# Performance work log

Hardware: AMD Instinct MI355X
Metric: run time of the kernel (lower is better)

The kernel has to match this reference:

```python
import jax, jax.numpy as jnp
import numpy as np

B, NUM_HIDDENS, H, W = 32, 128, 64, 64
EMB_DIM = 64
NUM_EMB = 512
COMMITMENT_COST = 0.25


def setup_inputs() -> dict:
    key = jax.random.key(0)
    ks = jax.random.split(key, 5)
    return {
        "bottom_encoding": jax.random.normal(ks[0], (B, NUM_HIDDENS, H, W), jnp.float32),
        "pre_w": jax.random.normal(ks[1], (EMB_DIM, NUM_HIDDENS), jnp.float32) / np.sqrt(NUM_HIDDENS).astype(np.float32),
        "pre_b": jnp.zeros((EMB_DIM,), jnp.float32),
        "codebook": jax.random.uniform(ks[2], (NUM_EMB, EMB_DIM), jnp.float32, -1.0 / NUM_EMB, 1.0 / NUM_EMB),
        "post_w": jax.random.normal(ks[3], (NUM_HIDDENS, EMB_DIM), jnp.float32) / np.sqrt(EMB_DIM).astype(np.float32),
        "post_b": jnp.zeros((NUM_HIDDENS,), jnp.float32),
    }


def reference(bottom_encoding, pre_w, pre_b, codebook, post_w, post_b):
    # pre-VQ 1x1 conv: [B, num_hiddens, H, W] -> [B, emb_dim, H, W]
    x = jnp.einsum('bchw,oc->bohw', bottom_encoding, pre_w) + pre_b[None, :, None, None]
    # BCHW -> BHWC, flatten to [N, D]
    z = jnp.transpose(x, (0, 2, 3, 1))
    flat = z.reshape(-1, EMB_DIM)
    # squared euclidean distances to codebook: [N, K]
    dists = (jnp.sum(flat * flat, axis=1, keepdims=True)
             + jnp.sum(codebook * codebook, axis=1)[None, :]
             - 2.0 * flat @ codebook.T)
    idx = jnp.argmin(dists, axis=1)              # [N] int
    quantized = codebook[idx].reshape(z.shape)   # gather, [B, H, W, D]
    # VQ losses
    e_latent_loss = jnp.mean((jax.lax.stop_gradient(quantized) - z) ** 2)
    q_latent_loss = jnp.mean((quantized - jax.lax.stop_gradient(z)) ** 2)
    loss = q_latent_loss + COMMITMENT_COST * e_latent_loss
    # straight-through estimator
    quantized_st = z + jax.lax.stop_gradient(quantized - z)
    # perplexity of codebook usage
    counts = jnp.zeros((NUM_EMB,), jnp.float32).at[idx].add(1.0)
    avg_probs = counts / idx.shape[0]
    perplexity = jnp.exp(-jnp.sum(avg_probs * jnp.log(avg_probs + 1e-10)))
    # post-VQ 1x1 conv: [B, emb_dim, H, W] -> [B, num_hiddens, H, W]
    qc = jnp.transpose(quantized_st, (0, 3, 1, 2))
    global_decode = jnp.einsum('bchw,oc->bohw', qc, post_w) + post_b[None, :, None, None]
    indices = idx.reshape(B, H, W)
    return loss, global_decode, perplexity, indices
```

## Files before the change

kernel.cpp:

```cpp
#include <hip/hip_runtime.h>

typedef unsigned short u16;
typedef unsigned int u32;
typedef __attribute__((ext_vector_type(8))) short short8v;
typedef __attribute__((ext_vector_type(4))) float f32x4;

#define NPX   131072
#define CHN   128
#define HWN   4096
#define EMB   64
#define NCODE 512

#define WS_HIST 0
#define WS_LOSS 2048
#define WS_CC   4096
#define WS_PWT  8192
#define WS_IDX  40960
#define WS_DT   303104


#define MFMA(a, b, c) __builtin_amdgcn_mfma_f32_16x16x32_bf16((a), (b), (c), 0, 0, 0)

#define SPLIT3(V, HH, MM, LL) {                          \
  u32 zb_ = __float_as_uint(V);                          \
  HH = zb_ >> 16;                                        \
  float fh_ = __uint_as_float(HH << 16);                 \
  float r1_ = __fsub_rn((V), fh_);                       \
  MM = __float_as_uint(r1_) >> 16;                       \
  float fm_ = __uint_as_float(MM << 16);                 \
  float r2_ = __fsub_rn(r1_, fm_);                       \
  LL = __float_as_uint(r2_) >> 16; }

__device__ __forceinline__ float rec3(u32 hb, u32 mb, u32 lb) {
  return __fadd_rn(__fadd_rn(__uint_as_float(hb), __uint_as_float(mb)),
                   __uint_as_float(lb));
}

__global__ __launch_bounds__(512) void vq_prep(const float* __restrict__ preW,
                                               const float* __restrict__ cb,
                                               float* __restrict__ preWT,
                                               float* __restrict__ cc,
                                               u16* __restrict__ ch,
                                               u16* __restrict__ cm,
                                               u16* __restrict__ cl) {
  int t = threadIdx.x;
  for (int i = t; i < CHN * EMB; i += 512) {
    int c = i >> 6, d = i & 63;
    preWT[i] = preW[d * CHN + c];
  }
  if (t < NCODE) {
    const float* row = cb + t * EMB;
    float r[8];
#pragma unroll
    for (int j = 0; j < 8; ++j) r[j] = __fmul_rn(row[j], row[j]);
#pragma unroll
    for (int b = 1; b < 8; ++b)
#pragma unroll
      for (int j = 0; j < 8; ++j)
        r[j] = __fadd_rn(r[j], __fmul_rn(row[b * 8 + j], row[b * 8 + j]));
    cc[t] = __fadd_rn(__fadd_rn(__fadd_rn(r[0], r[1]), __fadd_rn(r[2], r[3])),
                      __fadd_rn(__fadd_rn(r[4], r[5]), __fadd_rn(r[6], r[7])));
    int tile = t >> 4, rr = t & 15;
    for (int d = 0; d < EMB; ++d) {
      float v = row[d];
      u32 hh, mm, ll;
      SPLIT3(v, hh, mm, ll)
      size_t ti = (size_t)tile * 1024 + (size_t)(d >> 3) * 128 + rr * 8 + (d & 7);
      ch[ti] = (u16)hh;
      cm[ti] = (u16)mm;
      cl[ti] = (u16)ll;
    }
  }
}

__global__ __launch_bounds__(256) void vq_dtab(const float* __restrict__ cb,
                                               const float* __restrict__ postW,
                                               const float* __restrict__ postB,
                                               float* __restrict__ DT) {
  int idx = blockIdx.x * 256 + threadIdx.x;
  int k = idx >> 7, o = idx & 127;
  const float* q = cb + k * EMB;
  const float* w = postW + o * EMB;
  float a0 = 0.f, a1 = 0.f, a2 = 0.f, a3 = 0.f;
#pragma unroll
  for (int dd = 0; dd < 64; dd += 4) {
    a0 = fmaf(q[dd + 0], w[dd + 0], a0);
    a1 = fmaf(q[dd + 1], w[dd + 1], a1);
    a2 = fmaf(q[dd + 2], w[dd + 2], a2);
    a3 = fmaf(q[dd + 3], w[dd + 3], a3);
  }
  DT[(size_t)k * 128 + o] = ((a0 + a1) + (a2 + a3)) + postB[o];
}

__global__ __launch_bounds__(256) void vq_pre(const float* __restrict__ A,
                                              const float* __restrict__ preWT,
                                              const float* __restrict__ preB,
                                              u16* __restrict__ zh,
                                              u16* __restrict__ zm,
                                              u16* __restrict__ zl) {
  int bid = blockIdx.x;
  int ph = bid & 511, dh = bid >> 9;
  int d0 = dh << 5;
  int p = ph * 256 + threadIdx.x;
  int b = p >> 12, hw = p & 4095;
  const float* Ab = A + (size_t)b * CHN * HWN + hw;

  float z[32];
#pragma unroll
  for (int d = 0; d < 32; ++d) z[d] = 0.f;
  for (int c = 0; c < CHN; c += 4) {
    float a0 = Ab[(size_t)(c + 0) * HWN];
    float a1 = Ab[(size_t)(c + 1) * HWN];
    float a2 = Ab[(size_t)(c + 2) * HWN];
    float a3 = Ab[(size_t)(c + 3) * HWN];
    const float* w = preWT + c * EMB + d0;
#pragma unroll
    for (int d = 0; d < 32; ++d) z[d] = __fadd_rn(z[d], __fmul_rn(a0, w[d]));
    w += EMB;
#pragma unroll
    for (int d = 0; d < 32; ++d) z[d] = __fadd_rn(z[d], __fmul_rn(a1, w[d]));
    w += EMB;
#pragma unroll
    for (int d = 0; d < 32; ++d) z[d] = __fadd_rn(z[d], __fmul_rn(a2, w[d]));
    w += EMB;
#pragma unroll
    for (int d = 0; d < 32; ++d) z[d] = __fadd_rn(z[d], __fmul_rn(a3, w[d]));
  }
#pragma unroll
  for (int d = 0; d < 32; ++d) z[d] = __fadd_rn(z[d], preB[d0 + d]);

  u32 hwd[16], mwd[16], lwd[16];
#pragma unroll
  for (int i = 0; i < 32; ++i) {
    u32 hh, mm, ll;
    SPLIT3(z[i], hh, mm, ll)
    int wdi = i >> 1;
    if ((i & 1) == 0) { hwd[wdi] = hh; mwd[wdi] = mm; lwd[wdi] = ll; }
    else { hwd[wdi] |= hh << 16; mwd[wdi] |= mm << 16; lwd[wdi] |= ll << 16; }
  }
  int tile = p >> 4, rr = p & 15;
  size_t base = (size_t)tile * 1024 + (size_t)(dh * 4) * 128 + rr * 8;
#pragma unroll
  for (int q = 0; q < 4; ++q) {
    size_t off = base + (size_t)q * 128;
    *(uint4*)(zh + off) = make_uint4(hwd[4*q], hwd[4*q+1], hwd[4*q+2], hwd[4*q+3]);
    *(uint4*)(zm + off) = make_uint4(mwd[4*q], mwd[4*q+1], mwd[4*q+2], mwd[4*q+3]);
    *(uint4*)(zl + off) = make_uint4(lwd[4*q], lwd[4*q+1], lwd[4*q+2], lwd[4*q+3]);
  }
}

__global__ __launch_bounds__(256) void vq_zz(const u16* __restrict__ zh,
                                             const u16* __restrict__ zm,
                                             const u16* __restrict__ zl,
                                             float* __restrict__ zz) {
  int p = blockIdx.x * 256 + threadIdx.x;
  int tile = p >> 4, rr = p & 15;
  size_t base = (size_t)tile * 1024 + rr * 8;
  float r[8];
#pragma unroll
  for (int bb = 0; bb < 8; ++bb) {
    size_t off = base + (size_t)bb * 128;
    uint4 h4 = *(const uint4*)(zh + off);
    uint4 m4 = *(const uint4*)(zm + off);
    uint4 l4 = *(const uint4*)(zl + off);
    float zv[8];
    zv[0] = rec3(h4.x << 16, m4.x << 16, l4.x << 16);
    zv[1] = rec3(h4.x & 0xffff0000u, m4.x & 0xffff0000u, l4.x & 0xffff0000u);
    zv[2] = rec3(h4.y << 16, m4.y << 16, l4.y << 16);
    zv[3] = rec3(h4.y & 0xffff0000u, m4.y & 0xffff0000u, l4.y & 0xffff0000u);
    zv[4] = rec3(h4.z << 16, m4.z << 16, l4.z << 16);
    zv[5] = rec3(h4.z & 0xffff0000u, m4.z & 0xffff0000u, l4.z & 0xffff0000u);
    zv[6] = rec3(h4.w << 16, m4.w << 16, l4.w << 16);
    zv[7] = rec3(h4.w & 0xffff0000u, m4.w & 0xffff0000u, l4.w & 0xffff0000u);
#pragma unroll
    for (int j = 0; j < 8; ++j) {
      float sq = __fmul_rn(zv[j], zv[j]);
      r[j] = (bb == 0) ? sq : __fadd_rn(r[j], sq);
    }
  }
  zz[p] = __fadd_rn(__fadd_rn(__fadd_rn(r[0], r[1]), __fadd_rn(r[2], r[3])),
                    __fadd_rn(__fadd_rn(r[4], r[5]), __fadd_rn(r[6], r[7])));
}


#define LOADB(S, T) {                                                   \
  size_t ob_ = (size_t)((T) & 31) * 1024 + l8;                          \
  S##h0 = *(const short8v*)(ch + ob_); S##h1 = *(const short8v*)(ch + ob_ + 512); \
  S##m0 = *(const short8v*)(cm + ob_); S##m1 = *(const short8v*)(cm + ob_ + 512); \
  S##l0 = *(const short8v*)(cl + ob_); S##l1 = *(const short8v*)(cl + ob_ + 512); }

#define COMP(S, T) {                                                    \
  float ccv_ = scc[((T) << 4) + mcol];                                  \
  _Pragma("unroll")                                                     \
  for (int mt = 0; mt < 4; ++mt) {                                      \
    f32x4 acc = {0.f, 0.f, 0.f, 0.f};                                   \
    acc = MFMA(Ah[mt][0], S##h0, acc); acc = MFMA(Ah[mt][1], S##h1, acc); \
    acc = MFMA(Am[mt][0], S##h0, acc); acc = MFMA(Am[mt][1], S##h1, acc); \
    acc = MFMA(Ah[mt][0], S##m0, acc); acc = MFMA(Ah[mt][1], S##m1, acc); \
    acc = MFMA(Am[mt][0], S##m0, acc); acc = MFMA(Am[mt][1], S##m1, acc); \
    acc = MFMA(Al[mt][0], S##h0, acc); acc = MFMA(Al[mt][1], S##h1, acc); \
    acc = MFMA(Ah[mt][0], S##l0, acc); acc = MFMA(Ah[mt][1], S##l1, acc); \
    acc = MFMA(Al[mt][0], S##m0, acc); acc = MFMA(Al[mt][1], S##m1, acc); \
    acc = MFMA(Am[mt][0], S##l0, acc); acc = MFMA(Am[mt][1], S##l1, acc); \
    _Pragma("unroll")                                                   \
    for (int r = 0; r < 4; ++r) {                                       \
      float dist_ = __fadd_rn(__fadd_rn(zzr[mt][r], ccv_), -2.0f * acc[r]); \
      if (dist_ < best[mt][r]) { best[mt][r] = dist_; bidx[mt][r] = ((T) << 4) + mcol; } \
    } } }

__global__ __launch_bounds__(256, 2) void vq_search(const u16* __restrict__ zh,
                                                    const u16* __restrict__ zm,
                                                    const u16* __restrict__ zl,
                                                    const u16* __restrict__ ch,
                                                    const u16* __restrict__ cm,
                                                    const u16* __restrict__ cl,
                                                    const float* __restrict__ cc,
                                                    const float* __restrict__ zz,
                                                    u16* __restrict__ wsIdx) {
  __shared__ float scc[512];
  int tid = threadIdx.x;
  scc[tid] = cc[tid];
  scc[tid + 256] = cc[tid + 256];
  __syncthreads();

  int lane = tid & 63, wid = tid >> 6;
  int Mbase = blockIdx.x * 256 + wid * 64;
  int mcol = lane & 15, g = lane >> 4;
  size_t l8 = (size_t)lane * 8;

  short8v Ah[4][2], Am[4][2], Al[4][2];
#pragma unroll
  for (int mt = 0; mt < 4; ++mt) {
    size_t tz = (size_t)((Mbase >> 4) + mt) * 1024 + l8;
    Ah[mt][0] = *(const short8v*)(zh + tz); Ah[mt][1] = *(const short8v*)(zh + tz + 512);
    Am[mt][0] = *(const short8v*)(zm + tz); Am[mt][1] = *(const short8v*)(zm + tz + 512);
    Al[mt][0] = *(const short8v*)(zl + tz); Al[mt][1] = *(const short8v*)(zl + tz + 512);
  }
  float zzr[4][4];
#pragma unroll
  for (int mt = 0; mt < 4; ++mt)
#pragma unroll
    for (int r = 0; r < 4; ++r)
      zzr[mt][r] = zz[Mbase + mt * 16 + g * 4 + r];

  float best[4][4];
  int bidx[4][4];
#pragma unroll
  for (int mt = 0; mt < 4; ++mt)
#pragma unroll
    for (int r = 0; r < 4; ++r) { best[mt][r] = 3.4e38f; bidx[mt][r] = 0; }

  short8v PAh0, PAh1, PAm0, PAm1, PAl0, PAl1;
  short8v PBh0, PBh1, PBm0, PBm1, PBl0, PBl1;
  LOADB(PA, 0)
#pragma unroll 1
  for (int t2 = 0; t2 < 16; ++t2) {
    int t = t2 * 2;
    LOADB(PB, t + 1)
    COMP(PA, t)
    LOADB(PA, t + 2)
    COMP(PB, t + 1)
  }

#pragma unroll
  for (int mt = 0; mt < 4; ++mt)
#pragma unroll
    for (int r = 0; r < 4; ++r) {
      float v = best[mt][r];
      int ix = bidx[mt][r];
#pragma unroll
      for (int off = 1; off < 16; off <<= 1) {
        float ov = __shfl_xor(v, off, 64);
        int oi = __shfl_xor(ix, off, 64);
        if (ov < v || (ov == v && oi < ix)) { v = ov; ix = oi; }
      }
      if (mcol == 0) wsIdx[Mbase + mt * 16 + g * 4 + r] = (u16)ix;
    }
}

__global__ __launch_bounds__(256) void vq_combine(const u16* __restrict__ zh,
                                                  const u16* __restrict__ zm,
                                                  const u16* __restrict__ zl,
                                                  const float* __restrict__ cb,
                                                  const u16* __restrict__ wsIdx,
                                                  float* __restrict__ outIdx,
                                                  float* __restrict__ lossAcc,
                                                  unsigned int* __restrict__ hist) {
  int p = blockIdx.x * 256 + threadIdx.x;
  int k = wsIdx[p];
  const float4* q4 = (const float4*)(cb + (k << 6));
  int tile = p >> 4, rr = p & 15;
  size_t base = (size_t)tile * 1024 + rr * 8;
  float ls = 0.f;
#pragma unroll
  for (int bb = 0; bb < 8; ++bb) {
    size_t off = base + (size_t)bb * 128;
    uint4 h4 = *(const uint4*)(zh + off);
    uint4 m4 = *(const uint4*)(zm + off);
    uint4 l4 = *(const uint4*)(zl + off);
    float4 qa = q4[2 * bb], qb = q4[2 * bb + 1];
    float z0 = rec3(h4.x << 16, m4.x << 16, l4.x << 16);
    float z1 = rec3(h4.x & 0xffff0000u, m4.x & 0xffff0000u, l4.x & 0xffff0000u);
    float z2 = rec3(h4.y << 16, m4.y << 16, l4.y << 16);
    float z3 = rec3(h4.y & 0xffff0000u, m4.y & 0xffff0000u, l4.y & 0xffff0000u);
    float z4v = rec3(h4.z << 16, m4.z << 16, l4.z << 16);
    float z5 = rec3(h4.z & 0xffff0000u, m4.z & 0xffff0000u, l4.z & 0xffff0000u);
    float z6 = rec3(h4.w << 16, m4.w << 16, l4.w << 16);
    float z7 = rec3(h4.w & 0xffff0000u, m4.w & 0xffff0000u, l4.w & 0xffff0000u);
    float e;
    e = __fsub_rn(qa.x, z0); ls = fmaf(e, e, ls);
    e = __fsub_rn(qa.y, z1); ls = fmaf(e, e, ls);
    e = __fsub_rn(qa.z, z2); ls = fmaf(e, e, ls);
    e = __fsub_rn(qa.w, z3); ls = fmaf(e, e, ls);
    e = __fsub_rn(qb.x, z4v); ls = fmaf(e, e, ls);
    e = __fsub_rn(qb.y, z5); ls = fmaf(e, e, ls);
    e = __fsub_rn(qb.z, z6); ls = fmaf(e, e, ls);
    e = __fsub_rn(qb.w, z7); ls = fmaf(e, e, ls);
  }
#pragma unroll
  for (int off = 32; off; off >>= 1) ls += __shfl_xor(ls, off, 64);
  if ((threadIdx.x & 63) == 0) atomicAdd(lossAcc, ls);
  atomicAdd(&hist[k], 1u);
  outIdx[p] = (float)k;
}

__global__ __launch_bounds__(256) void vq_decode(const u16* __restrict__ wsIdx,
                                                 const float* __restrict__ DT,
                                                 float* __restrict__ dec) {
  int p = blockIdx.x * 256 + threadIdx.x;
  int b = p >> 12, hw = p & 4095;
  int k = wsIdx[p];
  const float4* Dk = (const float4*)(DT + (size_t)k * 128);
  float* out = dec + (size_t)b * CHN * HWN + hw;
#pragma unroll 4
  for (int oq = 0; oq < 32; ++oq) {
    float4 v = Dk[oq];
    out[(size_t)(4 * oq + 0) * HWN] = v.x;
    out[(size_t)(4 * oq + 1) * HWN] = v.y;
    out[(size_t)(4 * oq + 2) * HWN] = v.z;
    out[(size_t)(4 * oq + 3) * HWN] = v.w;
  }
}

__global__ __launch_bounds__(512) void vq_final(const unsigned int* __restrict__ hist,
                                                const float* __restrict__ lossAcc,
                                                float* __restrict__ outLoss,
                                                float* __restrict__ outPerp) {
  __shared__ float sred[8];
  int t = threadIdx.x;
  float c = (float)hist[t];
  float pavg = c * (1.0f / 131072.0f);
  float term = pavg * logf(pavg + 1e-10f);
#pragma unroll
  for (int off = 32; off; off >>= 1) term += __shfl_xor(term, off, 64);
  if ((t & 63) == 0) sred[t >> 6] = term;
  __syncthreads();
  if (t == 0) {
    float s = 0.f;
    for (int i = 0; i < 8; ++i) s += sred[i];
    *outPerp = expf(-s);
    *outLoss = 1.25f * (*lossAcc) * (1.0f / 8388608.0f);
  }
}

extern "C" void kernel_launch(void* const* d_in, const int* in_sizes, int n_in,
                              void* d_out, int out_size, void* d_ws, size_t ws_size,
                              hipStream_t stream) {
  const float* A     = (const float*)d_in[0];
  const float* preW  = (const float*)d_in[1];
  const float* preB  = (const float*)d_in[2];
  const float* cb    = (const float*)d_in[3];
  const float* postW = (const float*)d_in[4];
  const float* postB = (const float*)d_in[5];
  float* out = (float*)d_out;

  char* ws = (char*)d_ws;
  unsigned int* hist = (unsigned int*)(ws + WS_HIST);
  float* lossAcc = (float*)(ws + WS_LOSS);
  float* cc      = (float*)(ws + WS_CC);
  float* preWT   = (float*)(ws + WS_PWT);
  u16* wsIdx     = (u16*)(ws + WS_IDX);
  float* DT      = (float*)(ws + WS_DT);

  char* outc = (char*)d_out;
  u16*   zh = (u16*)(outc + 32);
  u16*   zm = (u16*)(outc + 16777248);
  u16*   zl = (u16*)(outc + 33554464);
  float* zz = (float*)(outc + 50331680);
  u16*   ch = (u16*)(outc + 50855968);
  u16*   cm = (u16*)(outc + 50921504);
  u16*   cl = (u16*)(outc + 50987040);

  hipMemsetAsync(ws, 0, 2052, stream);
  vq_prep<<<1, 512, 0, stream>>>(preW, cb, preWT, cc, ch, cm, cl);
  vq_dtab<<<256, 256, 0, stream>>>(cb, postW, postB, DT);
  vq_pre<<<1024, 256, 0, stream>>>(A, preWT, preB, zh, zm, zl);
  vq_zz<<<512, 256, 0, stream>>>(zh, zm, zl, zz);
  vq_search<<<512, 256, 0, stream>>>(zh, zm, zl, ch, cm, cl, cc, zz, wsIdx);
  vq_combine<<<512, 256, 0, stream>>>(zh, zm, zl, cb, wsIdx,
                                      out + 16777218, lossAcc, hist);
  vq_decode<<<512, 256, 0, stream>>>(wsIdx, DT, out + 1);
  vq_final<<<1, 512, 0, stream>>>(hist, lossAcc, out, out + 16777217);
}
```

Baseline: 320.2 us.

## Fuse prep kernels, fold norm and loss into search, shrink per-wave tiles

Merges the prep, codebook-table and workspace-zeroing work into one init kernel, replacing the memset. The zz-norm and combine kernels are folded into the search kernel: z is rebuilt in shared memory from the split bf16 fragments, and norms, loss, histogram and index output are computed in place. Per-wave M tiles are halved, occupancy hints are raised, and the double-buffered codebook loads become a simple loop. vq_pre handles 16 channels per block with twice the blocks. This removes launches and re-reads of z, but adds shared-memory pressure and loses the explicit load/compute prefetch overlap.

```diff
diff --git a/kernel.cpp b/kernel.cpp
--- a/kernel.cpp
+++ b/kernel.cpp
@@ -36,60 +36,65 @@
                    __uint_as_float(lb));
 }
 
-__global__ __launch_bounds__(512) void vq_prep(const float* __restrict__ preW,
+__global__ __launch_bounds__(256) void vq_init(const float* __restrict__ preW,
                                                const float* __restrict__ cb,
+                                               const float* __restrict__ postW,
+                                               const float* __restrict__ postB,
                                                float* __restrict__ preWT,
                                                float* __restrict__ cc,
                                                u16* __restrict__ ch,
                                                u16* __restrict__ cm,
-                                               u16* __restrict__ cl) {
-  int t = threadIdx.x;
-  for (int i = t; i < CHN * EMB; i += 512) {
-    int c = i >> 6, d = i & 63;
-    preWT[i] = preW[d * CHN + c];
-  }
-  if (t < NCODE) {
-    const float* row = cb + t * EMB;
-    float r[8];
-#pragma unroll
-    for (int j = 0; j < 8; ++j) r[j] = __fmul_rn(row[j], row[j]);
-#pragma unroll
-    for (int b = 1; b < 8; ++b)
-#pragma unroll
-      for (int j = 0; j < 8; ++j)
-        r[j] = __fadd_rn(r[j], __fmul_rn(row[b * 8 + j], row[b * 8 + j]));
-    cc[t] = __fadd_rn(__fadd_rn(__fadd_rn(r[0], r[1]), __fadd_rn(r[2], r[3])),
-                      __fadd_rn(__fadd_rn(r[4], r[5]), __fadd_rn(r[6], r[7])));
-    int tile = t >> 4, rr = t & 15;
-    for (int d = 0; d < EMB; ++d) {
-      float v = row[d];
-      u32 hh, mm, ll;
-      SPLIT3(v, hh, mm, ll)
-      size_t ti = (size_t)tile * 1024 + (size_t)(d >> 3) * 128 + rr * 8 + (d & 7);
-      ch[ti] = (u16)hh;
-      cm[ti] = (u16)mm;
-      cl[ti] = (u16)ll;
-    }
-  }
-}
-
-__global__ __launch_bounds__(256) void vq_dtab(const float* __restrict__ cb,
-                                               const float* __restrict__ postW,
-                                               const float* __restrict__ postB,
-                                               float* __restrict__ DT) {
-  int idx = blockIdx.x * 256 + threadIdx.x;
-  int k = idx >> 7, o = idx & 127;
-  const float* q = cb + k * EMB;
-  const float* w = postW + o * EMB;
-  float a0 = 0.f, a1 = 0.f, a2 = 0.f, a3 = 0.f;
-#pragma unroll
-  for (int dd = 0; dd < 64; dd += 4) {
-    a0 = fmaf(q[dd + 0], w[dd + 0], a0);
-    a1 = fmaf(q[dd + 1], w[dd + 1], a1);
-    a2 = fmaf(q[dd + 2], w[dd + 2], a2);
-    a3 = fmaf(q[dd + 3], w[dd + 3], a3);
-  }
-  DT[(size_t)k * 128 + o] = ((a0 + a1) + (a2 + a3)) + postB[o];
+                                               u16* __restrict__ cl,
+                                               float* __restrict__ DT,
+                                               u32* __restrict__ wz) {
+  int bid = blockIdx.x, tid = threadIdx.x;
+  int idx = bid * 256 + tid;
+  {
+    int k = idx >> 7, o = idx & 127;
+    const float* q = cb + k * EMB;
+    const float* w = postW + o * EMB;
+    float a0 = 0.f, a1 = 0.f, a2 = 0.f, a3 = 0.f;
+#pragma unroll
+    for (int dd = 0; dd < 64; dd += 4) {
+      a0 = fmaf(q[dd + 0], w[dd + 0], a0);
+      a1 = fmaf(q[dd + 1], w[dd + 1], a1);
+      a2 = fmaf(q[dd + 2], w[dd + 2], a2);
+      a3 = fmaf(q[dd + 3], w[dd + 3], a3);
+    }
+    DT[(size_t)k * 128 + o] = ((a0 + a1) + (a2 + a3)) + postB[o];
+  }
+  if (bid == 0) {
+    for (int i = tid; i < CHN * EMB; i += 256) {
+      int c = i >> 6, d = i & 63;
+      preWT[i] = preW[d * CHN + c];
+    }
+  } else if (bid == 1) {
+    for (int t = tid; t < NCODE; t += 256) {
+      const float* row = cb + t * EMB;
+      float r[8];
+#pragma unroll
+      for (int j = 0; j < 8; ++j) r[j] = __fmul_rn(row[j], row[j]);
+#pragma unroll
+      for (int b = 1; b < 8; ++b)
+#pragma unroll
+        for (int j = 0; j < 8; ++j)
+          r[j] = __fadd_rn(r[j], __fmul_rn(row[b * 8 + j], row[b * 8 + j]));
+      cc[t] = __fadd_rn(__fadd_rn(__fadd_rn(r[0], r[1]), __fadd_rn(r[2], r[3])),
+                        __fadd_rn(__fadd_rn(r[4], r[5]), __fadd_rn(r[6], r[7])));
+      int tile = t >> 4, rr = t & 15;
+      for (int d = 0; d < EMB; ++d) {
+        float v = row[d];
+        u32 hh, mm, ll;
+        SPLIT3(v, hh, mm, ll)
+        size_t ti = (size_t)tile * 1024 + (size_t)(d >> 3) * 128 + rr * 8 + (d & 7);
+        ch[ti] = (u16)hh;
+        cm[ti] = (u16)mm;
+        cl[ti] = (u16)ll;
+      }
+    }
+  } else if (bid == 2) {
+    for (int i = tid; i < 513; i += 256) wz[i] = 0;
+  }
 }
 
 __global__ __launch_bounds__(256) void vq_pre(const float* __restrict__ A,
@@ -100,14 +105,14 @@
                                               u16* __restrict__ zl) {
   int bid = blockIdx.x;
   int ph = bid & 511, dh = bid >> 9;
-  int d0 = dh << 5;
+  int d0 = dh << 4;
   int p = ph * 256 + threadIdx.x;
   int b = p >> 12, hw = p & 4095;
   const float* Ab = A + (size_t)b * CHN * HWN + hw;
 
-  float z[32];
-#pragma unroll
-  for (int d = 0; d < 32; ++d) z[d] = 0.f;
+  float z[16];
+#pragma unroll
+  for (int d = 0; d < 16; ++d) z[d] = 0.f;
   for (int c = 0; c < CHN; c += 4) {
     float a0 = Ab[(size_t)(c + 0) * HWN];
     float a1 = Ab[(size_t)(c + 1) * HWN];
@@ -115,23 +120,23 @@
     float a3 = Ab[(size_t)(c + 3) * HWN];
     const float* w = preWT + c * EMB + d0;
 #pragma unroll
-    for (int d = 0; d < 32; ++d) z[d] = __fadd_rn(z[d], __fmul_rn(a0, w[d]));
+    for (int d = 0; d < 16; ++d) z[d] = __fadd_rn(z[d], __fmul_rn(a0, w[d]));
     w += EMB;
 #pragma unroll
-    for (int d = 0; d < 32; ++d) z[d] = __fadd_rn(z[d], __fmul_rn(a1, w[d]));
+    for (int d = 0; d < 16; ++d) z[d] = __fadd_rn(z[d], __fmul_rn(a1, w[d]));
     w += EMB;
 #pragma unroll
-    for (int d = 0; d < 32; ++d) z[d] = __fadd_rn(z[d], __fmul_rn(a2, w[d]));
+    for (int d = 0; d < 16; ++d) z[d] = __fadd_rn(z[d], __fmul_rn(a2, w[d]));
     w += EMB;
 #pragma unroll
-    for (int d = 0; d < 32; ++d) z[d] = __fadd_rn(z[d], __fmul_rn(a3, w[d]));
-  }
-#pragma unroll
-  for (int d = 0; d < 32; ++d) z[d] = __fadd_rn(z[d], preB[d0 + d]);
-
-  u32 hwd[16], mwd[16], lwd[16];
-#pragma unroll
-  for (int i = 0; i < 32; ++i) {
+    for (int d = 0; d < 16; ++d) z[d] = __fadd_rn(z[d], __fmul_rn(a3, w[d]));
+  }
+#pragma unroll
+  for (int d = 0; d < 16; ++d) z[d] = __fadd_rn(z[d], preB[d0 + d]);
+
+  u32 hwd[8], mwd[8], lwd[8];
+#pragma unroll
+  for (int i = 0; i < 16; ++i) {
     u32 hh, mm, ll;
     SPLIT3(z[i], hh, mm, ll)
     int wdi = i >> 1;
@@ -139,9 +144,9 @@
     else { hwd[wdi] |= hh << 16; mwd[wdi] |= mm << 16; lwd[wdi] |= ll << 16; }
   }
   int tile = p >> 4, rr = p & 15;
-  size_t base = (size_t)tile * 1024 + (size_t)(dh * 4) * 128 + rr * 8;
-#pragma unroll
-  for (int q = 0; q < 4; ++q) {
+  size_t base = (size_t)tile * 1024 + (size_t)(dh * 2) * 128 + rr * 8;
+#pragma unroll
+  for (int q = 0; q < 2; ++q) {
     size_t off = base + (size_t)q * 128;
     *(uint4*)(zh + off) = make_uint4(hwd[4*q], hwd[4*q+1], hwd[4*q+2], hwd[4*q+3]);
     *(uint4*)(zm + off) = make_uint4(mwd[4*q], mwd[4*q+1], mwd[4*q+2], mwd[4*q+3]);
@@ -149,121 +154,123 @@
   }
 }
 
-__global__ __launch_bounds__(256) void vq_zz(const u16* __restrict__ zh,
-                                             const u16* __restrict__ zm,
-                                             const u16* __restrict__ zl,
-                                             float* __restrict__ zz) {
-  int p = blockIdx.x * 256 + threadIdx.x;
-  int tile = p >> 4, rr = p & 15;
-  size_t base = (size_t)tile * 1024 + rr * 8;
-  float r[8];
-#pragma unroll
-  for (int bb = 0; bb < 8; ++bb) {
-    size_t off = base + (size_t)bb * 128;
-    uint4 h4 = *(const uint4*)(zh + off);
-    uint4 m4 = *(const uint4*)(zm + off);
-    uint4 l4 = *(const uint4*)(zl + off);
-    float zv[8];
-    zv[0] = rec3(h4.x << 16, m4.x << 16, l4.x << 16);
-    zv[1] = rec3(h4.x & 0xffff0000u, m4.x & 0xffff0000u, l4.x & 0xffff0000u);
-    zv[2] = rec3(h4.y << 16, m4.y << 16, l4.y << 16);
-    zv[3] = rec3(h4.y & 0xffff0000u, m4.y & 0xffff0000u, l4.y & 0xffff0000u);
-    zv[4] = rec3(h4.z << 16, m4.z << 16, l4.z << 16);
-    zv[5] = rec3(h4.z & 0xffff0000u, m4.z & 0xffff0000u, l4.z & 0xffff0000u);
-    zv[6] = rec3(h4.w << 16, m4.w << 16, l4.w << 16);
-    zv[7] = rec3(h4.w & 0xffff0000u, m4.w & 0xffff0000u, l4.w & 0xffff0000u);
-#pragma unroll
-    for (int j = 0; j < 8; ++j) {
-      float sq = __fmul_rn(zv[j], zv[j]);
-      r[j] = (bb == 0) ? sq : __fadd_rn(r[j], sq);
-    }
-  }
-  zz[p] = __fadd_rn(__fadd_rn(__fadd_rn(r[0], r[1]), __fadd_rn(r[2], r[3])),
-                    __fadd_rn(__fadd_rn(r[4], r[5]), __fadd_rn(r[6], r[7])));
-}
-
-
-#define LOADB(S, T) {                                                   \
-  size_t ob_ = (size_t)((T) & 31) * 1024 + l8;                          \
-  S##h0 = *(const short8v*)(ch + ob_); S##h1 = *(const short8v*)(ch + ob_ + 512); \
-  S##m0 = *(const short8v*)(cm + ob_); S##m1 = *(const short8v*)(cm + ob_ + 512); \
-  S##l0 = *(const short8v*)(cl + ob_); S##l1 = *(const short8v*)(cl + ob_ + 512); }
-
-#define COMP(S, T) {                                                    \
+
+#define LOADB(T) { size_t ob_ = (size_t)(T) * 1024 + l8;                         \
+  Bh0 = *(const short8v*)(ch + ob_); Bh1 = *(const short8v*)(ch + ob_ + 512);    \
+  Bm0 = *(const short8v*)(cm + ob_); Bm1 = *(const short8v*)(cm + ob_ + 512);    \
+  Bl0 = *(const short8v*)(cl + ob_); Bl1 = *(const short8v*)(cl + ob_ + 512); }
+
+#define COMP(T) {                                                       \
   float ccv_ = scc[((T) << 4) + mcol];                                  \
   _Pragma("unroll")                                                     \
-  for (int mt = 0; mt < 4; ++mt) {                                      \
+  for (int mt = 0; mt < 2; ++mt) {                                      \
     f32x4 acc = {0.f, 0.f, 0.f, 0.f};                                   \
-    acc = MFMA(Ah[mt][0], S##h0, acc); acc = MFMA(Ah[mt][1], S##h1, acc); \
-    acc = MFMA(Am[mt][0], S##h0, acc); acc = MFMA(Am[mt][1], S##h1, acc); \
-    acc = MFMA(Ah[mt][0], S##m0, acc); acc = MFMA(Ah[mt][1], S##m1, acc); \
-    acc = MFMA(Am[mt][0], S##m0, acc); acc = MFMA(Am[mt][1], S##m1, acc); \
-    acc = MFMA(Al[mt][0], S##h0, acc); acc = MFMA(Al[mt][1], S##h1, acc); \
-    acc = MFMA(Ah[mt][0], S##l0, acc); acc = MFMA(Ah[mt][1], S##l1, acc); \
-    acc = MFMA(Al[mt][0], S##m0, acc); acc = MFMA(Al[mt][1], S##m1, acc); \
-    acc = MFMA(Am[mt][0], S##l0, acc); acc = MFMA(Am[mt][1], S##l1, acc); \
+    acc = MFMA(Ah[mt][0], Bh0, acc); acc = MFMA(Ah[mt][1], Bh1, acc);   \
+    acc = MFMA(Am[mt][0], Bh0, acc); acc = MFMA(Am[mt][1], Bh1, acc);   \
+    acc = MFMA(Ah[mt][0], Bm0, acc); acc = MFMA(Ah[mt][1], Bm1, acc);   \
+    acc = MFMA(Am[mt][0], Bm0, acc); acc = MFMA(Am[mt][1], Bm1, acc);   \
+    acc = MFMA(Al[mt][0], Bh0, acc); acc = MFMA(Al[mt][1], Bh1, acc);   \
+    acc = MFMA(Ah[mt][0], Bl0, acc); acc = MFMA(Ah[mt][1], Bl1, acc);   \
+    acc = MFMA(Al[mt][0], Bm0, acc); acc = MFMA(Al[mt][1], Bm1, acc);   \
+    acc = MFMA(Am[mt][0], Bl0, acc); acc = MFMA(Am[mt][1], Bl1, acc);   \
     _Pragma("unroll")                                                   \
     for (int r = 0; r < 4; ++r) {                                       \
       float dist_ = __fadd_rn(__fadd_rn(zzr[mt][r], ccv_), -2.0f * acc[r]); \
       if (dist_ < best[mt][r]) { best[mt][r] = dist_; bidx[mt][r] = ((T) << 4) + mcol; } \
     } } }
 
-__global__ __launch_bounds__(256, 2) void vq_search(const u16* __restrict__ zh,
+__global__ __launch_bounds__(256, 4) void vq_search(const u16* __restrict__ zh,
                                                     const u16* __restrict__ zm,
                                                     const u16* __restrict__ zl,
                                                     const u16* __restrict__ ch,
                                                     const u16* __restrict__ cm,
                                                     const u16* __restrict__ cl,
                                                     const float* __restrict__ cc,
-                                                    const float* __restrict__ zz,
-                                                    u16* __restrict__ wsIdx) {
+                                                    const float* __restrict__ cb,
+                                                    u16* __restrict__ wsIdx,
+                                                    float* __restrict__ outIdx,
+                                                    float* __restrict__ lossAcc,
+                                                    unsigned int* __restrict__ hist) {
   __shared__ float scc[512];
+  __shared__ float zs[4][2][16][64];
+  __shared__ u16 kb[4][2][16];
   int tid = threadIdx.x;
   scc[tid] = cc[tid];
   scc[tid + 256] = cc[tid + 256];
-  __syncthreads();
 
   int lane = tid & 63, wid = tid >> 6;
-  int Mbase = blockIdx.x * 256 + wid * 64;
+  int Mbase = blockIdx.x * 128 + wid * 32;
   int mcol = lane & 15, g = lane >> 4;
   size_t l8 = (size_t)lane * 8;
 
-  short8v Ah[4][2], Am[4][2], Al[4][2];
-#pragma unroll
-  for (int mt = 0; mt < 4; ++mt) {
+  short8v Ah[2][2], Am[2][2], Al[2][2];
+#pragma unroll
+  for (int mt = 0; mt < 2; ++mt) {
     size_t tz = (size_t)((Mbase >> 4) + mt) * 1024 + l8;
     Ah[mt][0] = *(const short8v*)(zh + tz); Ah[mt][1] = *(const short8v*)(zh + tz + 512);
     Am[mt][0] = *(const short8v*)(zm + tz); Am[mt][1] = *(const short8v*)(zm + tz + 512);
     Al[mt][0] = *(const short8v*)(zl + tz); Al[mt][1] = *(const short8v*)(zl + tz + 512);
   }
-  float zzr[4][4];
-#pragma unroll
-  for (int mt = 0; mt < 4; ++mt)
-#pragma unroll
-    for (int r = 0; r < 4; ++r)
-      zzr[mt][r] = zz[Mbase + mt * 16 + g * 4 + r];
-
-  float best[4][4];
-  int bidx[4][4];
-#pragma unroll
-  for (int mt = 0; mt < 4; ++mt)
+#pragma unroll
+  for (int mt = 0; mt < 2; ++mt)
+#pragma unroll
+    for (int e = 0; e < 8; ++e) {
+      zs[wid][mt][mcol][g * 8 + e] =
+          rec3(((u32)(u16)Ah[mt][0][e]) << 16, ((u32)(u16)Am[mt][0][e]) << 16,
+               ((u32)(u16)Al[mt][0][e]) << 16);
+      zs[wid][mt][mcol][32 + g * 8 + e] =
+          rec3(((u32)(u16)Ah[mt][1][e]) << 16, ((u32)(u16)Am[mt][1][e]) << 16,
+               ((u32)(u16)Al[mt][1][e]) << 16);
+    }
+  __syncthreads();
+
+  float zzr[2][4];
+#pragma unroll
+  for (int mt = 0; mt < 2; ++mt)
+#pragma unroll
+    for (int r = 0; r < 4; ++r) {
+      const float* rowp = &zs[wid][mt][g * 4 + r][0];
+      float4 v0 = *(const float4*)(rowp);
+      float4 v1 = *(const float4*)(rowp + 4);
+      float4 a0, a1;
+      a0.x = __fmul_rn(v0.x, v0.x); a0.y = __fmul_rn(v0.y, v0.y);
+      a0.z = __fmul_rn(v0.z, v0.z); a0.w = __fmul_rn(v0.w, v0.w);
+      a1.x = __fmul_rn(v1.x, v1.x); a1.y = __fmul_rn(v1.y, v1.y);
+      a1.z = __fmul_rn(v1.z, v1.z); a1.w = __fmul_rn(v1.w, v1.w);
+#pragma unroll
+      for (int bb = 1; bb < 8; ++bb) {
+        v0 = *(const float4*)(rowp + bb * 8);
+        v1 = *(const float4*)(rowp + bb * 8 + 4);
+        a0.x = __fadd_rn(a0.x, __fmul_rn(v0.x, v0.x));
+        a0.y = __fadd_rn(a0.y, __fmul_rn(v0.y, v0.y));
+        a0.z = __fadd_rn(a0.z, __fmul_rn(v0.z, v0.z));
+        a0.w = __fadd_rn(a0.w, __fmul_rn(v0.w, v0.w));
+        a1.x = __fadd_rn(a1.x, __fmul_rn(v1.x, v1.x));
+        a1.y = __fadd_rn(a1.y, __fmul_rn(v1.y, v1.y));
+        a1.z = __fadd_rn(a1.z, __fmul_rn(v1.z, v1.z));
+        a1.w = __fadd_rn(a1.w, __fmul_rn(v1.w, v1.w));
+      }
+      zzr[mt][r] = __fadd_rn(
+          __fadd_rn(__fadd_rn(a0.x, a0.y), __fadd_rn(a0.z, a0.w)),
+          __fadd_rn(__fadd_rn(a1.x, a1.y), __fadd_rn(a1.z, a1.w)));
+    }
+
+  float best[2][4];
+  int bidx[2][4];
+#pragma unroll
+  for (int mt = 0; mt < 2; ++mt)
 #pragma unroll
     for (int r = 0; r < 4; ++r) { best[mt][r] = 3.4e38f; bidx[mt][r] = 0; }
 
-  short8v PAh0, PAh1, PAm0, PAm1, PAl0, PAl1;
-  short8v PBh0, PBh1, PBm0, PBm1, PBl0, PBl1;
-  LOADB(PA, 0)
-#pragma unroll 1
-  for (int t2 = 0; t2 < 16; ++t2) {
-    int t = t2 * 2;
-    LOADB(PB, t + 1)
-    COMP(PA, t)
-    LOADB(PA, t + 2)
-    COMP(PB, t + 1)
-  }
-
-#pragma unroll
-  for (int mt = 0; mt < 4; ++mt)
+  short8v Bh0, Bh1, Bm0, Bm1, Bl0, Bl1;
+#pragma unroll 2
+  for (int t = 0; t < 32; ++t) {
+    LOADB(t)
+    COMP(t)
+  }
+
+#pragma unroll
+  for (int mt = 0; mt < 2; ++mt)
 #pragma unroll
     for (int r = 0; r < 4; ++r) {
       float v = best[mt][r];
@@ -274,54 +281,39 @@
         int oi = __shfl_xor(ix, off, 64);
         if (ov < v || (ov == v && oi < ix)) { v = ov; ix = oi; }
       }
-      if (mcol == 0) wsIdx[Mbase + mt * 16 + g * 4 + r] = (u16)ix;
-    }
-}
-
-__global__ __launch_bounds__(256) void vq_combine(const u16* __restrict__ zh,
-                                                  const u16* __restrict__ zm,
-                                                  const u16* __restrict__ zl,
-                                                  const float* __restrict__ cb,
-                                                  const u16* __restrict__ wsIdx,
-                                                  float* __restrict__ outIdx,
-                                                  float* __restrict__ lossAcc,
-                                                  unsigned int* __restrict__ hist) {
-  int p = blockIdx.x * 256 + threadIdx.x;
-  int k = wsIdx[p];
-  const float4* q4 = (const float4*)(cb + (k << 6));
-  int tile = p >> 4, rr = p & 15;
-  size_t base = (size_t)tile * 1024 + rr * 8;
+      if (mcol == 0) {
+        int row = Mbase + mt * 16 + g * 4 + r;
+        wsIdx[row] = (u16)ix;
+        outIdx[row] = (float)ix;
+        kb[wid][mt][g * 4 + r] = (u16)ix;
+        atomicAdd(&hist[ix], 1u);
+      }
+    }
+  __syncthreads();
+
   float ls = 0.f;
-#pragma unroll
-  for (int bb = 0; bb < 8; ++bb) {
-    size_t off = base + (size_t)bb * 128;
-    uint4 h4 = *(const uint4*)(zh + off);
-    uint4 m4 = *(const uint4*)(zm + off);
-    uint4 l4 = *(const uint4*)(zl + off);
-    float4 qa = q4[2 * bb], qb = q4[2 * bb + 1];
-    float z0 = rec3(h4.x << 16, m4.x << 16, l4.x << 16);
-    float z1 = rec3(h4.x & 0xffff0000u, m4.x & 0xffff0000u, l4.x & 0xffff0000u);
-    float z2 = rec3(h4.y << 16, m4.y << 16, l4.y << 16);
-    float z3 = rec3(h4.y & 0xffff0000u, m4.y & 0xffff0000u, l4.y & 0xffff0000u);
-    float z4v = rec3(h4.z << 16, m4.z << 16, l4.z << 16);
-    float z5 = rec3(h4.z & 0xffff0000u, m4.z & 0xffff0000u, l4.z & 0xffff0000u);
-    float z6 = rec3(h4.w << 16, m4.w << 16, l4.w << 16);
-    float z7 = rec3(h4.w & 0xffff0000u, m4.w & 0xffff0000u, l4.w & 0xffff0000u);
-    float e;
-    e = __fsub_rn(qa.x, z0); ls = fmaf(e, e, ls);
-    e = __fsub_rn(qa.y, z1); ls = fmaf(e, e, ls);
-    e = __fsub_rn(qa.z, z2); ls = fmaf(e, e, ls);
-    e = __fsub_rn(qa.w, z3); ls = fmaf(e, e, ls);
-    e = __fsub_rn(qb.x, z4v); ls = fmaf(e, e, ls);
-    e = __fsub_rn(qb.y, z5); ls = fmaf(e, e, ls);
-    e = __fsub_rn(qb.z, z6); ls = fmaf(e, e, ls);
-    e = __fsub_rn(qb.w, z7); ls = fmaf(e, e, ls);
+  if (lane < 32) {
+    int mt = lane >> 4, row = lane & 15;
+    int krow = kb[wid][mt][row];
+    const float4* q4 = (const float4*)(cb + (krow << 6));
+    const float* zrow = &zs[wid][mt][row][0];
+#pragma unroll
+    for (int bb = 0; bb < 8; ++bb) {
+      float4 qa = q4[2 * bb], qb = q4[2 * bb + 1];
+      float e;
+      e = __fsub_rn(qa.x, zrow[8 * bb + 0]); ls = fmaf(e, e, ls);
+      e = __fsub_rn(qa.y, zrow[8 * bb + 1]); ls = fmaf(e, e, ls);
+      e = __fsub_rn(qa.z, zrow[8 * bb + 2]); ls = fmaf(e, e, ls);
+      e = __fsub_rn(qa.w, zrow[8 * bb + 3]); ls = fmaf(e, e, ls);
+      e = __fsub_rn(qb.x, zrow[8 * bb + 4]); ls = fmaf(e, e, ls);
+      e = __fsub_rn(qb.y, zrow[8 * bb + 5]); ls = fmaf(e, e, ls);
+      e = __fsub_rn(qb.z, zrow[8 * bb + 6]); ls = fmaf(e, e, ls);
+      e = __fsub_rn(qb.w, zrow[8 * bb + 7]); ls = fmaf(e, e, ls);
+    }
   }
 #pragma unroll
   for (int off = 32; off; off >>= 1) ls += __shfl_xor(ls, off, 64);
-  if ((threadIdx.x & 63) == 0) atomicAdd(lossAcc, ls);
-  atomicAdd(&hist[k], 1u);
-  outIdx[p] = (float)k;
+  if (lane == 0) atomicAdd(lossAcc, ls);
 }
 
 __global__ __launch_bounds__(256) void vq_decode(const u16* __restrict__ wsIdx,
@@ -383,22 +375,18 @@
   float* DT      = (float*)(ws + WS_DT);
 
   char* outc = (char*)d_out;
-  u16*   zh = (u16*)(outc + 32);
-  u16*   zm = (u16*)(outc + 16777248);
-  u16*   zl = (u16*)(outc + 33554464);
-  float* zz = (float*)(outc + 50331680);
-  u16*   ch = (u16*)(outc + 50855968);
-  u16*   cm = (u16*)(outc + 50921504);
-  u16*   cl = (u16*)(outc + 50987040);
-
-  hipMemsetAsync(ws, 0, 2052, stream);
-  vq_prep<<<1, 512, 0, stream>>>(preW, cb, preWT, cc, ch, cm, cl);
-  vq_dtab<<<256, 256, 0, stream>>>(cb, postW, postB, DT);
-  vq_pre<<<1024, 256, 0, stream>>>(A, preWT, preB, zh, zm, zl);
-  vq_zz<<<512, 256, 0, stream>>>(zh, zm, zl, zz);
-  vq_search<<<512, 256, 0, stream>>>(zh, zm, zl, ch, cm, cl, cc, zz, wsIdx);
-  vq_combine<<<512, 256, 0, stream>>>(zh, zm, zl, cb, wsIdx,
-                                      out + 16777218, lossAcc, hist);
+  u16* zh = (u16*)(outc + 32);
+  u16* zm = (u16*)(outc + 16777248);
+  u16* zl = (u16*)(outc + 33554464);
+  u16* ch = (u16*)(outc + 50855968);
+  u16* cm = (u16*)(outc + 50921504);
+  u16* cl = (u16*)(outc + 50987040);
+
+  vq_init<<<256, 256, 0, stream>>>(preW, cb, postW, postB, preWT, cc,
+                                   ch, cm, cl, DT, (u32*)ws);
+  vq_pre<<<2048, 256, 0, stream>>>(A, preWT, preB, zh, zm, zl);
+  vq_search<<<1024, 256, 0, stream>>>(zh, zm, zl, ch, cm, cl, cc, cb,
+                                      wsIdx, out + 16777218, lossAcc, hist);
   vq_decode<<<512, 256, 0, stream>>>(wsIdx, DT, out + 1);
   vq_final<<<1, 512, 0, stream>>>(hist, lossAcc, out, out + 16777217);
 }
```

New measurement: 326.7 us. 2.0% more time.
